# Performance work log

Measured on AMD Instinct MI355X. Metric: run time of the kernel, lower is better.

The kernel has to match this reference:

```python
import jax, jax.numpy as jnp
import numpy as np

D = 256      # d_model
SUB = 3      # number of adjacency subsets
GROUPS = 8
N, T, V = 32, 256, 19


def setup_inputs() -> dict:
    key = jax.random.key(0)
    ks = jax.random.split(key, 4)
    return {
        "x": jax.random.normal(ks[0], (N, T, V, D), jnp.float32),
        "para": jax.random.normal(ks[1], (3, GROUPS, V, V), jnp.float32),
        "linear_weight": jax.random.normal(ks[2], (D, D * SUB), jnp.float32) * 0.05,
        "linear_bias": jax.random.normal(ks[3], (1, D * SUB, 1, 1), jnp.float32) * 0.05,
        "bn_gamma": jnp.ones((D * SUB,), jnp.float32),
        "bn_beta": jnp.zeros((D * SUB,), jnp.float32),
        "bn1_gamma": jnp.ones((D,), jnp.float32),
        "bn1_beta": jnp.zeros((D,), jnp.float32),
    }


def _bn(x, gamma, beta, eps=1e-5):
    # BatchNorm2d (training mode): stats over (n, t, v) per channel
    m = jnp.mean(x, axis=(0, 2, 3), keepdims=True)
    v = jnp.var(x, axis=(0, 2, 3), keepdims=True)
    return (x - m) * jax.lax.rsqrt(v + eps) * gamma[None, :, None, None] + beta[None, :, None, None]


def reference(x, para, linear_weight, linear_bias, bn_gamma, bn_beta, bn1_gamma, bn1_beta):
    xc = jnp.transpose(x, (0, 3, 1, 2))                 # (n, c, t, v)
    # expand per-group adjacency to per-channel: (3, D, V, V)
    A = jnp.tile(para, (1, D // GROUPS, 1, 1))
    # L2 row-normalize along last dim (matches torch.norm(dim=-1))
    A = A / (jnp.linalg.norm(A, axis=-1, keepdims=True) + 1e-4)
    # channel mixing: (n, 3c, t, v)
    y = jnp.einsum('nctw,cd->ndtw', xc, linear_weight)
    y = _bn(y + linear_bias, bn_gamma, bn_beta)
    n, kc, t, v = y.shape
    y = y.reshape(n, SUB, kc // SUB, t, v)              # (n, k, c, t, v)
    # per-channel tiny 19x19 adjacency matmul
    y = jnp.einsum('nkctv,kcvw->nctw', y, A)            # (n, c, t, v)
    out = jax.nn.relu(_bn(y + xc, bn1_gamma, bn1_beta))
    return jnp.transpose(out, (0, 2, 3, 1))             # (n, t, v, c)
```

## Files before the change

kernel.cpp:

```cpp
#include <hip/hip_runtime.h>

typedef unsigned short u16;
typedef unsigned int u32;
typedef float f32x4 __attribute__((ext_vector_type(4)));
typedef __bf16 bf16x8 __attribute__((ext_vector_type(8)));

#define M_ALL 155648.0f
#define GP 168

__device__ __forceinline__ u16 f2bf(float f) {
  union { float f; u32 u; } x; x.f = f;
  u32 u = x.u;
  u += 0x7FFFu + ((u >> 16) & 1u);
  return (u16)(u >> 16);
}
__device__ __forceinline__ float bf2f(u16 h) {
  union { u32 u; float f; } x; x.u = ((u32)h) << 16;
  return x.f;
}
__device__ __forceinline__ f32x4 zero4() { f32x4 z = {0.f, 0.f, 0.f, 0.f}; return z; }

__device__ __forceinline__ int xs_idx(int m, int c) {
  return m * 256 + ((((c >> 3) ^ (m & 7)) << 3) | (c & 7));
}
__device__ __forceinline__ int y2_idx(int r, int kvp) {
  int sw = (r & 7) ^ ((r >> 3) & 7);
  return r * 64 + ((((kvp >> 3) ^ sw) << 3) | (kvp & 7));
}

__global__ void k_prep(const float* __restrict__ para, u16* __restrict__ wa2) {
  __shared__ float aL[3 * 8 * 19 * 19];
  int tid = threadIdx.x;
  if (tid < 456) {
    int k = tid / 152, rem = tid % 152, g = rem / 19, v = rem % 19;
    int base = ((k * 8 + g) * 19 + v) * 19;
    float ss = 0.f;
    #pragma unroll
    for (int w = 0; w < 19; ++w) { float a = para[base + w]; ss += a * a; }
    float inv = 1.f / (sqrtf(ss) + 1e-4f);
    #pragma unroll
    for (int w = 0; w < 19; ++w) aL[base + w] = para[base + w] * inv;
  }
  __syncthreads();
  for (int i = tid; i < 8 * 20 * 64; i += 512) {
    int g = i / 1280, rem = i % 1280, w = rem >> 6, kvp = rem & 63;
    u16 val = 0;
    if (w < 19 && kvp < 57) {
      int k = kvp / 19, v = kvp - 19 * k;
      val = f2bf(aL[((k * 8 + g) * 19 + v) * 19 + w]);
    }
    wa2[i] = val;
  }
}

__global__ void k_wt(const float* __restrict__ W, u16* __restrict__ wt) {
  int idx = blockIdx.x * 512 + threadIdx.x;
  int d = idx >> 8, c = idx & 255;
  wt[idx] = f2bf(W[c * 768 + d]);
}

__global__ __launch_bounds__(512) void k_cvt(const float* __restrict__ x,
                                             u16* __restrict__ xbf,
                                             float* __restrict__ colsum) {
  __shared__ float scs[2048];
  int tid = threadIdx.x;
  float p0 = 0.f, p1 = 0.f, p2 = 0.f, p3 = 0.f;
  const float4* x4 = reinterpret_cast<const float4*>(x);
  ushort4* o4 = reinterpret_cast<ushort4*>(xbf);
  #pragma unroll 1
  for (size_t idx = (size_t)blockIdx.x * 512 + tid; idx < 9961472u; idx += 524288u) {
    float4 f = x4[idx];
    ushort4 o;
    o.x = f2bf(f.x); o.y = f2bf(f.y); o.z = f2bf(f.z); o.w = f2bf(f.w);
    o4[idx] = o;
    p0 += f.x; p1 += f.y; p2 += f.z; p3 += f.w;
  }
  int c4 = tid & 63, w8 = tid >> 6;
  scs[w8 * 256 + c4 * 4 + 0] = p0;
  scs[w8 * 256 + c4 * 4 + 1] = p1;
  scs[w8 * 256 + c4 * 4 + 2] = p2;
  scs[w8 * 256 + c4 * 4 + 3] = p3;
  __syncthreads();
  if (tid < 256) {
    float s = 0.f;
    #pragma unroll
    for (int h = 0; h < 8; ++h) s += scs[h * 256 + tid];
    atomicAdd(&colsum[tid], s);
  }
}

template<int BF>
__global__ __launch_bounds__(512, 2) void k_gram(const float* __restrict__ x,
                                                 const u16* __restrict__ xbf,
                                                 float* __restrict__ Gp,
                                                 float* __restrict__ colsum) {
  __shared__ u16 xsT[256 * GP];
  __shared__ float scs[512];
  int tid = threadIdx.x, bid = blockIdx.x;
  int c = tid & 255, mh = tid >> 8;
  int lane = tid & 63, wave = tid >> 6;
  int cl = lane & 15, q = lane >> 4;

  if (tid < 256) {
    *reinterpret_cast<uint2*>(&xsT[tid * GP + 152]) = make_uint2(0u, 0u);
    *reinterpret_cast<uint2*>(&xsT[tid * GP + 156]) = make_uint2(0u, 0u);
  }

  float cs = 0.f;
  f32x4 acc[2][16];
  #pragma unroll
  for (int ri = 0; ri < 2; ++ri)
    #pragma unroll
    for (int j = 0; j < 16; ++j) acc[ri][j] = zero4();

  for (int ss = 0; ss < 4; ++ss) {
    int sl = bid * 4 + ss;
    __syncthreads();
    if constexpr (BF) {
      const u16* xb16 = xbf + (size_t)sl * 152 * 256;
      #pragma unroll 4
      for (int it = 0; it < 19; ++it) {
        int m0 = it * 8 + mh * 4;
        u32 v0 = xb16[(m0 + 0) * 256 + c];
        u32 v1 = xb16[(m0 + 1) * 256 + c];
        u32 v2 = xb16[(m0 + 2) * 256 + c];
        u32 v3 = xb16[(m0 + 3) * 256 + c];
        uint2 p;
        p.x = v0 | (v1 << 16);
        p.y = v2 | (v3 << 16);
        *reinterpret_cast<uint2*>(&xsT[c * GP + m0]) = p;
      }
    } else {
      const float* xb = x + (size_t)sl * 152 * 256;
      #pragma unroll 1
      for (int it = 0; it < 19; ++it) {
        int m0 = it * 8 + mh * 4;
        float v0 = xb[(m0 + 0) * 256 + c];
        float v1 = xb[(m0 + 1) * 256 + c];
        float v2 = xb[(m0 + 2) * 256 + c];
        float v3 = xb[(m0 + 3) * 256 + c];
        cs += v0 + v1 + v2 + v3;
        uint2 p;
        p.x = (u32)f2bf(v0) | ((u32)f2bf(v1) << 16);
        p.y = (u32)f2bf(v2) | ((u32)f2bf(v3) << 16);
        *reinterpret_cast<uint2*>(&xsT[c * GP + m0]) = p;
      }
    }
    __syncthreads();
    #pragma unroll
    for (int s = 0; s < 5; ++s) {
      int kof = s * 32 + q * 8;
      bf16x8 a0 = *reinterpret_cast<const bf16x8*>(&xsT[(wave * 16 + cl) * GP + kof]);
      bf16x8 a1 = *reinterpret_cast<const bf16x8*>(&xsT[((wave + 8) * 16 + cl) * GP + kof]);
      #pragma unroll
      for (int ct2 = 0; ct2 < 16; ++ct2) {
        bf16x8 b = *reinterpret_cast<const bf16x8*>(&xsT[(ct2 * 16 + cl) * GP + kof]);
        acc[0][ct2] = __builtin_amdgcn_mfma_f32_16x16x32_bf16(a0, b, acc[0][ct2], 0, 0, 0);
        acc[1][ct2] = __builtin_amdgcn_mfma_f32_16x16x32_bf16(a1, b, acc[1][ct2], 0, 0, 0);
      }
    }
  }
  #pragma unroll
  for (int ri = 0; ri < 2; ++ri) {
    int ct = wave + ri * 8;
    int tb = 16 * ct - (ct * (ct - 1)) / 2 - ct;
    #pragma unroll
    for (int ct2 = 0; ct2 < 16; ++ct2) {
      if (ct2 >= ct) {
        float* dst = Gp + ((size_t)(tb + ct2) * 256 + bid) * 256;
        #pragma unroll
        for (int r4 = 0; r4 < 4; ++r4)
          dst[(q * 4 + r4) * 16 + cl] = acc[ri][ct2][r4];
      }
    }
  }
  if constexpr (!BF) {
    scs[tid] = cs;
    __syncthreads();
    if (tid < 256) atomicAdd(&colsum[tid], scs[tid] + scs[tid + 256]);
  }
}

__global__ __launch_bounds__(256) void k_red(const float* __restrict__ Gp,
                                             float* __restrict__ G) {
  int b = blockIdx.x;
  int e = threadIdx.x;
  int ct = 0;
  #pragma unroll
  for (int t = 1; t < 16; ++t)
    if (b >= 16 * t - (t * (t - 1)) / 2) ct = t;
  int ct2 = ct + (b - (16 * ct - (ct * (ct - 1)) / 2));
  const float* src = Gp + (size_t)b * 65536;
  float s = 0.f;
  #pragma unroll 8
  for (int p = 0; p < 256; ++p) s += src[p * 256 + e];
  int row = e >> 4, col = e & 15;
  int rr = ct * 16 + row, cc = ct2 * 16 + col;
  G[rr * 256 + cc] = s;
  G[cc * 256 + rr] = s;
}

__global__ __launch_bounds__(256) void k_f1(const float* __restrict__ G,
                                            const float* __restrict__ colsum,
                                            const float* __restrict__ W,
                                            const float* __restrict__ gam,
                                            const float* __restrict__ bet,
                                            float* __restrict__ ST) {
  __shared__ float wd[256];
  __shared__ float red[16];
  int d = blockIdx.x, c = threadIdx.x;
  float wv = W[c * 768 + d];
  wd[c] = wv;
  __syncthreads();
  float dot = 0.f;
  const float* Gr = G + c * 256;
  #pragma unroll 4
  for (int j = 0; j < 256; ++j) dot += Gr[j] * wd[j];
  float part = wv * dot;
  float mpart = colsum[c] * wv;
  #pragma unroll
  for (int o = 32; o; o >>= 1) { part += __shfl_down(part, o); mpart += __shfl_down(mpart, o); }
  int lane = c & 63, w = c >> 6;
  if (lane == 0) { red[w] = part; red[8 + w] = mpart; }
  __syncthreads();
  if (c == 0) {
    float qv = red[0] + red[1] + red[2] + red[3];
    float ms = red[8] + red[9] + red[10] + red[11];
    float mean = ms / M_ALL;
    float var = qv / M_ALL - mean * mean;
    float S = gam[d] * rsqrtf(var + 1e-5f);
    ST[d] = S;
    ST[768 + d] = bet[d] - mean * S;
  }
}

template<int BF>
__global__ __launch_bounds__(512, 2) void k_main(const float* __restrict__ x,
                                                 const u16* __restrict__ xbf,
                                                 const u16* __restrict__ wt,
                                                 const u16* __restrict__ wa2,
                                                 const float* __restrict__ ST,
                                                 float* __restrict__ sumz,
                                                 float* __restrict__ out) {
  __shared__ u16 xs[152 * 256];
  __shared__ u16 y2[512 * 64];
  __shared__ float scrz[1024];
  int tid = threadIdx.x;
  int bid = blockIdx.x;
  size_t obase = (size_t)bid * 152 * 256;

  if constexpr (BF) {
    const u16* xb16 = xbf + (size_t)bid * 152 * 256;
    int w = tid >> 6, lane = tid & 63;
    int ch = lane & 31, half = lane >> 5;
    for (int it = 0; it < 10; ++it) {
      int m = it * 16 + 2 * w + half;
      if (m < 152) {
        const u16* src = xb16 + m * 256 + ((ch ^ (m & 7)) << 3);
        *reinterpret_cast<bf16x8*>(&xs[m * 256 + (ch << 3)]) =
            *reinterpret_cast<const bf16x8*>(src);
      }
    }
  } else {
    const float* xbase = x + (size_t)bid * 152 * 256;
    int r = tid >> 6, c4 = (tid & 63) << 2;
    for (int it = 0; it < 19; ++it) {
      int m = it * 8 + r;
      float4 f = *reinterpret_cast<const float4*>(xbase + m * 256 + c4);
      uint2 p;
      p.x = (u32)f2bf(f.x) | ((u32)f2bf(f.y) << 16);
      p.y = (u32)f2bf(f.z) | ((u32)f2bf(f.w) << 16);
      *reinterpret_cast<uint2*>(&xs[xs_idx(m, c4)]) = p;
    }
  }

  int lane = tid & 63, wave = tid >> 6;
  int mhalf = wave & 1, nt3 = wave >> 1;
  int cl = lane & 15, q = lane >> 4;
  int g = wave;
  const bf16x8* wtv = reinterpret_cast<const bf16x8*>(wt);
  float* zbufF = reinterpret_cast<float*>(y2);

  bf16x8 bfr[2][2];
  #pragma unroll
  for (int ks = 0; ks < 2; ++ks)
    #pragma unroll
    for (int nt = 0; nt < 2; ++nt) {
      int w = nt * 16 + cl; int wc = (w < 20) ? w : 19;
      bfr[ks][nt] = *reinterpret_cast<const bf16x8*>(&wa2[(g * 20 + wc) * 64 + ks * 32 + q * 8]);
    }

  int arow[5], mlow[5];
  #pragma unroll
  for (int i = 0; i < 5; ++i) {
    int rr = mhalf * 80 + i * 16 + cl;
    if (rr > 151) rr = 151;
    arow[i] = rr * 256; mlow[i] = rr & 7;
  }
  __syncthreads();

  for (int nc = 0; nc < 4; ++nc) {
    f32x4 acc[5][3];
    #pragma unroll
    for (int i = 0; i < 5; ++i)
      #pragma unroll
      for (int jj = 0; jj < 3; ++jj) acc[i][jj] = zero4();
    for (int s = 0; s < 8; ++s) {
      int sq4 = s * 4 + q;
      bf16x8 b[3];
      #pragma unroll
      for (int jj = 0; jj < 3; ++jj) {
        int j = nt3 * 3 + jj;
        int d = (j >> 2) * 256 + nc * 64 + (j & 3) * 16 + cl;
        b[jj] = wtv[d * 32 + sq4];
      }
      #pragma unroll
      for (int i = 0; i < 5; ++i) {
        bf16x8 a = *reinterpret_cast<const bf16x8*>(&xs[arow[i] + ((sq4 ^ mlow[i]) << 3)]);
        #pragma unroll
        for (int jj = 0; jj < 3; ++jj)
          acc[i][jj] = __builtin_amdgcn_mfma_f32_16x16x32_bf16(a, b[jj], acc[i][jj], 0, 0, 0);
      }
    }
    __syncthreads();

    #pragma unroll
    for (int kk = 0; kk < 7; ++kk)
      y2[y2_idx(tid, 57 + kk)] = 0;

    #pragma unroll
    for (int jj = 0; jj < 3; ++jj) {
      int j = nt3 * 3 + jj;
      int ksub = j >> 2;
      int c_local = (j & 3) * 16 + cl;
      int d = ksub * 256 + nc * 64 + c_local;
      float Sc = ST[d], Tc = ST[768 + d];
      #pragma unroll
      for (int i = 0; i < 5; ++i) {
        int mb = mhalf * 80 + i * 16 + q * 4;
        #pragma unroll
        for (int r4 = 0; r4 < 4; ++r4) {
          int m = mb + r4;
          if (m < 152) {
            int t = (m * 27) >> 9;
            int v = m - t * 19;
            int kvp = ksub * 19 + v;
            int r = t * 64 + c_local;
            y2[y2_idx(r, kvp)] = f2bf(acc[i][jj][r4] * Sc + Tc);
          }
        }
      }
    }
    __syncthreads();

    f32x4 zacc[4][2];
    #pragma unroll
    for (int mt = 0; mt < 4; ++mt) { zacc[mt][0] = zero4(); zacc[mt][1] = zero4(); }
    #pragma unroll
    for (int ks = 0; ks < 2; ++ks) {
      #pragma unroll
      for (int mt = 0; mt < 4; ++mt) {
        int tc = mt * 16 + cl;
        int t = tc >> 3, c8 = tc & 7;
        int r = t * 64 + c8 * 8 + g;
        int ch = (ks * 4 + q) ^ g ^ c8;
        bf16x8 afr = *reinterpret_cast<const bf16x8*>(&y2[r * 64 + (ch << 3)]);
        #pragma unroll
        for (int nt = 0; nt < 2; ++nt)
          zacc[mt][nt] = __builtin_amdgcn_mfma_f32_16x16x32_bf16(afr, bfr[ks][nt], zacc[mt][nt], 0, 0, 0);
      }
    }
    __syncthreads();

    #pragma unroll
    for (int mt = 0; mt < 4; ++mt)
      #pragma unroll
      for (int nt = 0; nt < 2; ++nt) {
        int w = nt * 16 + cl;
        if (w < 19) {
          #pragma unroll
          for (int r4 = 0; r4 < 4; ++r4) {
            int mm = mt * 16 + q * 4 + r4;
            int t = mm >> 3, c8 = mm & 7;
            zbufF[(c8 * 8 + g) * 153 + t * 19 + w] = zacc[mt][nt][r4];
          }
        }
      }
    __syncthreads();

    float sz = 0.f, sq = 0.f;
    int cloc = tid & 63;
    int cglob = nc * 64 + cloc;
    #pragma unroll 1
    for (int rep = 0; rep < 19; ++rep) {
      int mp = rep * 8 + (tid >> 6);
      float z = zbufF[cloc * 153 + mp] + bf2f(xs[xs_idx(mp, cglob)]);
      out[obase + (size_t)mp * 256 + cglob] = z;
      sz += z; sq += z * z;
    }
    scrz[(tid >> 6) * 64 + cloc] = sz;
    scrz[512 + (tid >> 6) * 64 + cloc] = sq;
    __syncthreads();
    if (tid < 128) {
      int comp = tid >> 6, c = tid & 63;
      float v = 0.f;
      #pragma unroll
      for (int h = 0; h < 8; ++h) v += scrz[comp * 512 + h * 64 + c];
      atomicAdd(&sumz[comp * 256 + nc * 64 + c], v);
    }
  }
}

__global__ void k_f2(const float* __restrict__ statz, const float* __restrict__ gam,
                     const float* __restrict__ bet, float* __restrict__ S1T1) {
  int c = threadIdx.x;
  float inv = 1.f / M_ALL;
  float mz = statz[c] * inv;
  float qv = statz[256 + c] * inv;
  float var = qv - mz * mz;
  float Sc = gam[c] * rsqrtf(var + 1e-5f);
  S1T1[c] = Sc;
  S1T1[256 + c] = bet[c] - mz * Sc;
}

__global__ __launch_bounds__(256) void k_relu(float* __restrict__ out,
                                              const float* __restrict__ S1T1) {
  int tid = threadIdx.x;
  int lane = tid & 63;
  int wv = ((blockIdx.x << 8) + tid) >> 6;
  const float4* s14 = reinterpret_cast<const float4*>(S1T1);
  float4 sv = s14[lane], tv = s14[64 + lane];
  float4* o4 = reinterpret_cast<float4*>(out);
  #pragma unroll 1
  for (int r = 0; r < 19; ++r) {
    size_t i = ((size_t)r * 8192 + wv) * 64 + lane;
    float4 f = o4[i];
    f.x = fmaxf(f.x * sv.x + tv.x, 0.f);
    f.y = fmaxf(f.y * sv.y + tv.y, 0.f);
    f.z = fmaxf(f.z * sv.z + tv.z, 0.f);
    f.w = fmaxf(f.w * sv.w + tv.w, 0.f);
    o4[i] = f;
  }
}

extern "C" void kernel_launch(void* const* d_in, const int* in_sizes, int n_in,
                              void* d_out, int out_size, void* d_ws, size_t ws_size,
                              hipStream_t stream) {
  const float* x    = (const float*)d_in[0];
  const float* para = (const float*)d_in[1];
  const float* W    = (const float*)d_in[2];
  const float* bng  = (const float*)d_in[4];
  const float* bnb  = (const float*)d_in[5];
  const float* bn1g = (const float*)d_in[6];
  const float* bn1b = (const float*)d_in[7];
  float* out = (float*)d_out;

  char* ws = (char*)d_ws;
  u16* wt     = (u16*)ws;
  u16* wa2    = (u16*)(ws + 393216);
  float* G    = (float*)(ws + 413696);
  float* csum = (float*)(ws + 675840);
  float* sumz = (float*)(ws + 676864);
  float* ST   = (float*)(ws + 678912);
  float* S1T1 = (float*)(ws + 685056);
  u16* xbf    = (u16*)(ws + 687104);
  float* Gp   = (float*)d_out;

  const size_t NEED = 687104u + 79691776u;

  hipMemsetAsync(ws + 675840, 0, 1024 + 2048, stream);
  k_prep<<<dim3(1),    dim3(512), 0, stream>>>(para, wa2);
  k_wt  <<<dim3(384),  dim3(512), 0, stream>>>(W, wt);
  if (ws_size >= NEED) {
    k_cvt <<<dim3(1024), dim3(512), 0, stream>>>(x, xbf, csum);
    k_gram<1><<<dim3(256),  dim3(512), 0, stream>>>(x, xbf, Gp, csum);
    k_red <<<dim3(136),  dim3(256), 0, stream>>>(Gp, G);
    k_f1  <<<dim3(768),  dim3(256), 0, stream>>>(G, csum, W, bng, bnb, ST);
    k_main<1><<<dim3(1024), dim3(512), 0, stream>>>(x, xbf, wt, wa2, ST, sumz, out);
  } else {
    k_gram<0><<<dim3(256),  dim3(512), 0, stream>>>(x, nullptr, Gp, csum);
    k_red <<<dim3(136),  dim3(256), 0, stream>>>(Gp, G);
    k_f1  <<<dim3(768),  dim3(256), 0, stream>>>(G, csum, W, bng, bnb, ST);
    k_main<0><<<dim3(1024), dim3(512), 0, stream>>>(x, nullptr, wt, wa2, ST, sumz, out);
  }
  k_f2  <<<dim3(1),    dim3(256), 0, stream>>>(sumz, bn1g, bn1b, S1T1);
  k_relu<<<dim3(2048), dim3(256), 0, stream>>>(out, S1T1);
}
```

Measured before the change: 613.9 us.

## Write channel-major bf16 transpose in conversion kernel for Gram staging

The conversion kernel now also writes a channel-major (transposed) bf16 copy of x into the output buffer, using a shared-memory tile. The Gram kernel then loads contiguous 16-byte vectors per channel instead of strided 2-byte gathers across rows. Column sums are now computed from bf16-rounded values rather than fp32, which slightly changes precision, and the kernel writes an extra full-size tensor (about 80 MB) of traffic.

```diff
diff --git a/kernel.cpp b/kernel.cpp
--- a/kernel.cpp
+++ b/kernel.cpp
@@ -59,39 +59,50 @@
   wt[idx] = f2bf(W[c * 768 + d]);
 }
 
-__global__ __launch_bounds__(512) void k_cvt(const float* __restrict__ x,
-                                             u16* __restrict__ xbf,
-                                             float* __restrict__ colsum) {
-  __shared__ float scs[2048];
-  int tid = threadIdx.x;
-  float p0 = 0.f, p1 = 0.f, p2 = 0.f, p3 = 0.f;
-  const float4* x4 = reinterpret_cast<const float4*>(x);
-  ushort4* o4 = reinterpret_cast<ushort4*>(xbf);
+__global__ __launch_bounds__(256) void k_tr(const float* __restrict__ x,
+                                            u16* __restrict__ xbf,
+                                            u16* __restrict__ xT,
+                                            float* __restrict__ colsum) {
+  __shared__ u16 tl[256 * 64];
+  __shared__ float csl[256];
+  int t = threadIdx.x;
+  int l = t & 63, w = t >> 6;
+  size_t m0 = (size_t)blockIdx.x * 64;
+  int m = (int)m0 + l;
+  const float4* xr = reinterpret_cast<const float4*>(x + (size_t)m * 256);
   #pragma unroll 1
-  for (size_t idx = (size_t)blockIdx.x * 512 + tid; idx < 9961472u; idx += 524288u) {
-    float4 f = x4[idx];
-    ushort4 o;
-    o.x = f2bf(f.x); o.y = f2bf(f.y); o.z = f2bf(f.z); o.w = f2bf(f.w);
-    o4[idx] = o;
-    p0 += f.x; p1 += f.y; p2 += f.z; p3 += f.w;
-  }
-  int c4 = tid & 63, w8 = tid >> 6;
-  scs[w8 * 256 + c4 * 4 + 0] = p0;
-  scs[w8 * 256 + c4 * 4 + 1] = p1;
-  scs[w8 * 256 + c4 * 4 + 2] = p2;
-  scs[w8 * 256 + c4 * 4 + 3] = p3;
-  __syncthreads();
-  if (tid < 256) {
+  for (int it = 0; it < 16; ++it) {
+    int c4 = 4 * w + 16 * it;
+    float4 f = xr[c4 >> 2];
+    u16 b0 = f2bf(f.x), b1 = f2bf(f.y), b2 = f2bf(f.z), b3 = f2bf(f.w);
+    ushort4 pk; pk.x = b0; pk.y = b1; pk.z = b2; pk.w = b3;
+    *reinterpret_cast<ushort4*>(xbf + (size_t)m * 256 + c4) = pk;
+    tl[(c4 + 0) * 64 + l] = b0;
+    tl[(c4 + 1) * 64 + l] = b1;
+    tl[(c4 + 2) * 64 + l] = b2;
+    tl[(c4 + 3) * 64 + l] = b3;
+  }
+  __syncthreads();
+  #pragma unroll 1
+  for (int pass = 0; pass < 8; ++pass) {
+    int c = (t >> 3) + 32 * pass;
+    int g = t & 7;
+    bf16x8 v = *reinterpret_cast<const bf16x8*>(&tl[c * 64 + g * 8]);
+    *reinterpret_cast<bf16x8*>(&xT[(size_t)c * 155648 + m0 + g * 8]) = v;
+    union { bf16x8 v8; u16 u[8]; } uv; uv.v8 = v;
     float s = 0.f;
     #pragma unroll
-    for (int h = 0; h < 8; ++h) s += scs[h * 256 + tid];
-    atomicAdd(&colsum[tid], s);
-  }
+    for (int j = 0; j < 8; ++j) s += bf2f(uv.u[j]);
+    s += __shfl_down(s, 4); s += __shfl_down(s, 2); s += __shfl_down(s, 1);
+    if (g == 0) csl[c] = s;
+  }
+  __syncthreads();
+  atomicAdd(&colsum[t], csl[t]);
 }
 
 template<int BF>
 __global__ __launch_bounds__(512, 2) void k_gram(const float* __restrict__ x,
-                                                 const u16* __restrict__ xbf,
+                                                 const u16* __restrict__ xT,
                                                  float* __restrict__ Gp,
                                                  float* __restrict__ colsum) {
   __shared__ u16 xsT[256 * GP];
@@ -117,18 +128,12 @@
     int sl = bid * 4 + ss;
     __syncthreads();
     if constexpr (BF) {
-      const u16* xb16 = xbf + (size_t)sl * 152 * 256;
-      #pragma unroll 4
-      for (int it = 0; it < 19; ++it) {
-        int m0 = it * 8 + mh * 4;
-        u32 v0 = xb16[(m0 + 0) * 256 + c];
-        u32 v1 = xb16[(m0 + 1) * 256 + c];
-        u32 v2 = xb16[(m0 + 2) * 256 + c];
-        u32 v3 = xb16[(m0 + 3) * 256 + c];
-        uint2 p;
-        p.x = v0 | (v1 << 16);
-        p.y = v2 | (v3 << 16);
-        *reinterpret_cast<uint2*>(&xsT[c * GP + m0]) = p;
+      const u16* xc = xT + (size_t)bid * 608 + ss * 152;
+      #pragma unroll 1
+      for (int i = tid; i < 4864; i += 512) {
+        int cc = i / 19, g = i - cc * 19;
+        *reinterpret_cast<bf16x8*>(&xsT[cc * GP + g * 8]) =
+            *reinterpret_cast<const bf16x8*>(&xc[(size_t)cc * 155648 + g * 8]);
       }
     } else {
       const float* xb = x + (size_t)sl * 152 * 256;
@@ -464,7 +469,8 @@
   float* ST   = (float*)(ws + 678912);
   float* S1T1 = (float*)(ws + 685056);
   u16* xbf    = (u16*)(ws + 687104);
-  float* Gp   = (float*)d_out;
+  u16* xT   = (u16*)d_out;
+  float* Gp = (float*)((char*)d_out + 79691776);
 
   const size_t NEED = 687104u + 79691776u;
 
@@ -472,14 +478,15 @@
   k_prep<<<dim3(1),    dim3(512), 0, stream>>>(para, wa2);
   k_wt  <<<dim3(384),  dim3(512), 0, stream>>>(W, wt);
   if (ws_size >= NEED) {
-    k_cvt <<<dim3(1024), dim3(512), 0, stream>>>(x, xbf, csum);
-    k_gram<1><<<dim3(256),  dim3(512), 0, stream>>>(x, xbf, Gp, csum);
+    k_tr  <<<dim3(2432), dim3(256), 0, stream>>>(x, xbf, xT, csum);
+    k_gram<1><<<dim3(256),  dim3(512), 0, stream>>>(x, xT, Gp, csum);
     k_red <<<dim3(136),  dim3(256), 0, stream>>>(Gp, G);
     k_f1  <<<dim3(768),  dim3(256), 0, stream>>>(G, csum, W, bng, bnb, ST);
     k_main<1><<<dim3(1024), dim3(512), 0, stream>>>(x, xbf, wt, wa2, ST, sumz, out);
   } else {
-    k_gram<0><<<dim3(256),  dim3(512), 0, stream>>>(x, nullptr, Gp, csum);
-    k_red <<<dim3(136),  dim3(256), 0, stream>>>(Gp, G);
+    float* Gp0 = (float*)d_out;
+    k_gram<0><<<dim3(256),  dim3(512), 0, stream>>>(x, nullptr, Gp0, csum);
+    k_red <<<dim3(136),  dim3(256), 0, stream>>>(Gp0, G);
     k_f1  <<<dim3(768),  dim3(256), 0, stream>>>(G, csum, W, bng, bnb, ST);
     k_main<0><<<dim3(1024), dim3(512), 0, stream>>>(x, nullptr, wt, wa2, ST, sumz, out);
   }
```

New measurement: 763.9 us. 24.4% more time.
